# Performance work log

Hardware: AMD Instinct MI355X
Metric: run time of the kernel (lower is better)

The kernel has to match this reference:

```python
import jax, jax.numpy as jnp
import numpy as np

N_U, N_R, D, H, E = 100000, 50000, 128, 64, 1000000


def setup_inputs() -> dict:
    key = jax.random.key(0)
    ks = jax.random.split(key, 12)
    s = 1.0 / np.sqrt(D)
    return {
        "x_user": jax.random.normal(ks[0], (N_U, D), jnp.float32),
        "x_res": jax.random.normal(ks[1], (N_R, D), jnp.float32),
        "edge_ua_src": jax.random.randint(ks[2], (E,), 0, N_U),
        "edge_ua_dst": jax.random.randint(ks[3], (E,), 0, N_R),
        "edge_ru_src": jax.random.randint(ks[4], (E,), 0, N_R),
        "edge_ru_dst": jax.random.randint(ks[5], (E,), 0, N_U),
        "W_l_ua": jax.random.normal(ks[6], (D, H), jnp.float32) * s,
        "b_ua": jax.random.normal(ks[7], (H,), jnp.float32) * s,
        "W_r_ua": jax.random.normal(ks[8], (D, H), jnp.float32) * s,
        "W_l_ru": jax.random.normal(ks[9], (D, H), jnp.float32) * s,
        "b_ru": jax.random.normal(ks[10], (H,), jnp.float32) * s,
        "W_r_ru": jax.random.normal(ks[11], (D, H), jnp.float32) * s,
    }


def _sage(x_src, x_dst, src, dst, n_dst, W_l, b_l, W_r):
    # gather neighbor feats, scatter-mean onto dst nodes (0 for isolated nodes)
    agg = jax.ops.segment_sum(x_src[src], dst, num_segments=n_dst)  # [n_dst, D]
    cnt = jax.ops.segment_sum(jnp.ones((src.shape[0], 1), x_src.dtype), dst,
                              num_segments=n_dst)
    mean = agg / jnp.maximum(cnt, 1.0)
    # SAGEConv: lin_l(mean neighbor) + bias + lin_r(self), no bias on lin_r
    return mean @ W_l + b_l + x_dst @ W_r


def reference(x_user, x_res, edge_ua_src, edge_ua_dst, edge_ru_src, edge_ru_dst,
              W_l_ua, b_ua, W_r_ua, W_l_ru, b_ru, W_r_ru):
    out_res = jax.nn.relu(_sage(x_user, x_res, edge_ua_src, edge_ua_dst, N_R,
                                W_l_ua, b_ua, W_r_ua))
    out_user = jax.nn.relu(_sage(x_res, x_user, edge_ru_src, edge_ru_dst, N_U,
                                 W_l_ru, b_ru, W_r_ru))
    return out_user, out_res
```

## Files before the change

### kernel.cpp

```cpp
#include <hip/hip_runtime.h>

#define N_U 100000
#define N_R 50000
#define DIM 128
#define HID 64
#define NE  1000000

#define BROWS 128
#define NB_R ((N_R + 127) / 128)
#define NB_U ((N_U + 127) / 128)
#define NBKT (NB_R + NB_U)
#define N_TOT (N_R + N_U)
#define MAXB 800
#define CHUNK 4096
#define BINGRID ((NE + CHUNK - 1) / CHUNK)
#define NBIN (2 * BINGRID)
#define CAPR 3072
#define CAPU 1536
#define RCAP 48
#define GU2 ((N_U + 127) / 128)
#define GR2 ((N_R + 127) / 128)
#define NPROJ (GU2 + GR2)
#define NPREP (NBIN + NPROJ)
#define TRIPLE (3 * NBIN)
#define LDSU 9856
#define NGATH (2 * NB_R + 2 * NB_U)

typedef unsigned int uint;
typedef __attribute__((ext_vector_type(8))) short      bf16x8;
typedef __attribute__((ext_vector_type(4))) float      f32x4;
typedef __attribute__((ext_vector_type(2))) float      f32x2;
typedef __attribute__((ext_vector_type(8))) unsigned short u16x8;

__device__ inline uint bf16_rne(float f) {
    uint u = __float_as_uint(f);
    u += 0x7FFFu + ((u >> 16) & 1u);
    return u >> 16;
}
__device__ inline float bf_lo(uint v) { return __uint_as_float(v << 16); }
__device__ inline float bf_hi(uint v) { return __uint_as_float(v & 0xFFFF0000u); }

__device__ inline uint cvt_pk_bf16(float lo, float hi) {
    uint r;
    asm("v_cvt_pk_bf16_f32 %0, %1, %2" : "=v"(r) : "v"(lo), "v"(hi));
    return r;
}

__device__ inline void pk_acc(f32x2& acc, uint v) {
    f32x2 val;
    val[0] = __uint_as_float(v << 16);
    val[1] = __uint_as_float(v & 0xFFFF0000u);
    asm("v_pk_add_f32 %0, %1, %2" : "+v"(acc) : "v"(val));
}

__device__ inline int bucket_base(int b) {
    return (b < NB_R) ? b * CAPR : NB_R * CAPR + (b - NB_R) * CAPU;
}

__global__ __launch_bounds__(256) void wcvt_kernel(
    const float* __restrict__ Wlua, const float* __restrict__ Wlru,
    const float* __restrict__ Wrua, const float* __restrict__ Wrru,
    unsigned short* __restrict__ Wbf, int* __restrict__ cur)
{
    if (blockIdx.x < 4) {
        const float* Ws[4] = {Wlua, Wlru, Wrua, Wrru};
        const float* W = Ws[blockIdx.x];
        unsigned short* dst = Wbf + blockIdx.x * 8192;
        for (int i = threadIdx.x; i < 1024; i += 256) {
            int k8 = i >> 6, col = i & 63;
            u16x8 p;
#pragma unroll
            for (int j = 0; j < 8; ++j)
                p[j] = (unsigned short)bf16_rne(W[(k8 * 8 + j) * HID + col]);
            *(u16x8*)&dst[i * 8] = p;
        }
    } else {
        int i = (blockIdx.x - 4) * 256 + threadIdx.x;
        if (i < NBKT) cur[i] = 0;
    }
}

__global__ __launch_bounds__(512, 4) void prep_kernel(
    const int* __restrict__ srcA, const int* __restrict__ dstA,
    const int* __restrict__ srcB, const int* __restrict__ dstB,
    int* __restrict__ cur, int* __restrict__ rec,
    const float* __restrict__ xu, const float* __restrict__ xr,
    const unsigned short* __restrict__ Wbf,
    const float* __restrict__ b_ua, const float* __restrict__ b_ru,
    uint* __restrict__ h_user, uint* __restrict__ h_res,
    uint* __restrict__ sbuf)
{
    __shared__ __align__(16) uint lds[LDSU];

    const int bid = blockIdx.x;
    const int t = threadIdx.x;
    int binid = -1, projid = -1;
    if (bid < TRIPLE) {
        if (bid % 3 == 0) binid = bid / 3;
        else projid = (bid / 3) * 2 + (bid % 3 - 1);
    } else {
        projid = 2 * NBIN + (bid - TRIPLE);
    }

    if (binid >= 0) {
        int* cntL = (int*)lds;
        int* offL = cntL + MAXB;
        int* curL = offL + MAXB;
        int* gbase = curL + MAXB;
        int* srec = gbase + MAXB;
        unsigned short* sbkt = (unsigned short*)(lds + 7296);
        int* tmp = (int*)(lds + 9344);

        const int seg = (binid >= BINGRID) ? 1 : 0;
        const int blk = binid - seg * BINGRID;
        const int* __restrict__ src = seg ? srcB : srcA;
        const int* __restrict__ dst = seg ? dstB : dstA;
        const int nbkt   = seg ? NB_U : NB_R;
        const int bktOff = seg ? NB_R : 0;

        const int e0 = blk * CHUNK;
        const int nhere = min(CHUNK, NE - e0);

        for (int i = t; i < nbkt; i += 512) cntL[i] = 0;
        __syncthreads();

        int myB[8], myR[8];
#pragma unroll
        for (int l = 0; l < 8; ++l) {
            int i = e0 + l * 512 + t;
            if (i < NE) {
                int d = dst[i];
                myB[l] = d >> 7;
                myR[l] = ((d & 127) << 17) | src[i];
                atomicAdd(&cntL[myB[l]], 1);
            } else myB[l] = -1;
        }
        __syncthreads();

        int vals[4], s = 0;
#pragma unroll
        for (int l = 0; l < 4; ++l) {
            int idx = t * 4 + l;
            vals[l] = (idx < nbkt) ? cntL[idx] : 0;
            s += vals[l];
        }
        tmp[t] = s;
        __syncthreads();
        for (int o = 1; o < 512; o <<= 1) {
            int v = (t >= o) ? tmp[t - o] : 0;
            __syncthreads();
            tmp[t] += v;
            __syncthreads();
        }
        int run = tmp[t] - s;
#pragma unroll
        for (int l = 0; l < 4; ++l) {
            int idx = t * 4 + l;
            if (idx < nbkt) { offL[idx] = run; curL[idx] = run; }
            run += vals[l];
        }
        __syncthreads();

        for (int i = t; i < nbkt; i += 512)
            if (cntL[i] > 0)
                gbase[i] = bucket_base(bktOff + i) + atomicAdd(&cur[bktOff + i], cntL[i]);

#pragma unroll
        for (int l = 0; l < 8; ++l) {
            if (myB[l] >= 0) {
                int slot = atomicAdd(&curL[myB[l]], 1);
                srec[slot] = myR[l];
                sbkt[slot] = (unsigned short)myB[l];
            }
        }
        __syncthreads();

        for (int sI = t; sI < nhere; sI += 512) {
            int b = sbkt[sI];
            rec[gbase[b] + (sI - offL[b])] = srec[sI];
        }
        return;
    }

    int blk, nrows;
    const float *x, *bias;
    const unsigned short *w0g, *w1g;
    uint* hb; uint* sb;
    if (projid < GU2) {
        blk = projid; x = xu; w0g = Wbf; w1g = Wbf + 3 * 8192; bias = b_ru;
        hb = h_user; sb = sbuf; nrows = N_U;
    } else {
        blk = projid - GU2; x = xr; w0g = Wbf + 1 * 8192; w1g = Wbf + 2 * 8192;
        bias = b_ua; hb = h_res; sb = sbuf + (size_t)N_U * 32; nrows = N_R;
    }

    const int rowbase = blk * 128;

    {
        const uint4* s0 = (const uint4*)w0g;
        const uint4* s1 = (const uint4*)w1g;
        uint4* d0 = (uint4*)lds;
        uint4* d1 = (uint4*)(lds + 4096);
        for (int i = t; i < 1024; i += 512) { d0[i] = s0[i]; d1[i] = s1[i]; }
    }

    const int wv = t >> 6, l = t & 63;
    const int lrow = l & 15, lk = l >> 4;
    const int myrow = rowbase + wv * 16 + lrow;
    const bool valid = myrow < nrows;
    const float4* xp = (const float4*)(x + (size_t)myrow * DIM + lk * 8);

    float4 z = make_float4(0.f, 0.f, 0.f, 0.f);
    float4 x0a = z, x0b = z, x1a = z, x1b = z, x2a = z, x2b = z, x3a = z, x3b = z;
    if (valid) {
        x0a = xp[0];  x0b = xp[1];
        x1a = xp[8];  x1b = xp[9];
        x2a = xp[16]; x2b = xp[17];
        x3a = xp[24]; x3b = xp[25];
    }
    __syncthreads();

    f32x4 acc0[4], acc1[4];
#pragma unroll
    for (int n = 0; n < 4; ++n) { acc0[n] = (f32x4)0.f; acc1[n] = (f32x4)0.f; }

#define KKSTEP(KK, XA, XB)                                                        \
    {                                                                             \
        union { uint4 u; bf16x8 v; } af;                                          \
        af.u.x = cvt_pk_bf16(XA.x, XA.y);                                         \
        af.u.y = cvt_pk_bf16(XA.z, XA.w);                                         \
        af.u.z = cvt_pk_bf16(XB.x, XB.y);                                         \
        af.u.w = cvt_pk_bf16(XB.z, XB.w);                                         \
        const int k8 = KK * 4 + lk;                                               \
        _Pragma("unroll")                                                         \
        for (int n = 0; n < 4; ++n) {                                             \
            const int col = n * 16 + lrow;                                        \
            bf16x8 b0 = *(const bf16x8*)&lds[(k8 * 64 + col) * 4];                \
            bf16x8 b1 = *(const bf16x8*)&lds[4096 + (k8 * 64 + col) * 4];         \
            acc0[n] = __builtin_amdgcn_mfma_f32_16x16x32_bf16(af.v, b0, acc0[n], 0, 0, 0); \
            acc1[n] = __builtin_amdgcn_mfma_f32_16x16x32_bf16(af.v, b1, acc1[n], 0, 0, 0); \
        }                                                                         \
    }
    KKSTEP(0, x0a, x0b)
    KKSTEP(1, x1a, x1b)
    KKSTEP(2, x2a, x2b)
    KKSTEP(3, x3a, x3b)
#undef KKSTEP

#pragma unroll
    for (int n = 0; n < 4; ++n) {
        float bv = bias[n * 16 + lrow];
#pragma unroll
        for (int r = 0; r < 4; ++r) acc1[n][r] += bv;
    }

    __syncthreads();
    uint* hA = lds;
    uint* hS = lds + 4608;
#pragma unroll
    for (int n = 0; n < 4; ++n) {
#pragma unroll
        for (int r = 0; r < 4; ++r) {
            int row = wv * 16 + lk * 4 + r;
            float hm = acc0[n][r], ho = __shfl_xor(hm, 1);
            float sm = acc1[n][r], so = __shfl_xor(sm, 1);
            if (!(lrow & 1)) {
                int c2 = n * 8 + (lrow >> 1);
                hA[row * 36 + c2] = cvt_pk_bf16(hm, ho);
                hS[row * 36 + c2] = cvt_pk_bf16(sm, so);
            }
        }
    }
    __syncthreads();
    for (int i = t; i < 128 * 8; i += 512) {
        int r = i >> 3, q = i & 7;
        if (rowbase + r < nrows) {
            *(uint4*)(hb + (size_t)(rowbase + r) * 32 + q * 4) =
                *(const uint4*)&hA[r * 36 + q * 4];
            *(uint4*)(sb + (size_t)(rowbase + r) * 32 + q * 4) =
                *(const uint4*)&hS[r * 36 + q * 4];
        }
    }
}

__global__ __launch_bounds__(256) void csr_gather_kernel(
    const int* __restrict__ rec, const int* __restrict__ cur,
    const uint* __restrict__ hu, const uint* __restrict__ hr,
    const uint* __restrict__ sbuf, float* __restrict__ out)
{
    __shared__ int srecB[64 * RCAP];
    __shared__ int cntL[64];

    const int t = threadIdx.x;
    const int blk = blockIdx.x;
    int bkt, half, nrows;
    size_t rowOff;
    const uint* __restrict__ h;
    if (blk < 2 * NB_R) {
        bkt = blk >> 1; half = blk & 1;
        h = hu; rowOff = N_U; nrows = N_R;
    } else {
        int u = blk - 2 * NB_R;
        bkt = NB_R + (u >> 1); half = u & 1;
        h = hr; rowOff = 0; nrows = N_U;
    }
    const int lbase = ((bkt < NB_R) ? bkt * 128 : (bkt - NB_R) * 128) + half * 64;
    if (lbase >= nrows) return;

    const int rbase = bucket_base(bkt);
    const int rcnt  = min(cur[bkt], (bkt < NB_R) ? CAPR : CAPU);
    const int rlo   = half * 64;

    if (t < 64) cntL[t] = 0;
    __syncthreads();
    for (int i = t; i < rcnt; i += 256) {
        int r = rec[rbase + i];
        int lr = (r >> 17) - rlo;
        if ((unsigned)lr < 64u) {
            int slot = atomicAdd(&cntL[lr], 1);
            if (slot < RCAP) srecB[lr * RCAP + slot] = r;
        }
    }
    __syncthreads();

    const int team = t >> 5, l32 = t & 31;
    const int q  = l32 >> 3;
    const int cl = l32 & 7;

    for (int rr = team; rr < 64; rr += 8) {
        const int lr = lbase + rr;
        if (lr >= nrows) continue;
        const int d = min(cntL[rr], RCAP);
        const int base = rr * RCAP;
        const uint* srow = sbuf + (rowOff + lr) * 32;
        float* orow = out + (rowOff + lr) * 64;

        float s0 = 0.f, s1 = 0.f, s2 = 0.f, s3 = 0.f;
        float s4 = 0.f, s5 = 0.f, s6 = 0.f, s7 = 0.f;
        if (l32 < 8) {
            uint4 sv = *(const uint4*)(srow + cl * 4);
            s0 = bf_lo(sv.x); s1 = bf_hi(sv.x); s2 = bf_lo(sv.y); s3 = bf_hi(sv.y);
            s4 = bf_lo(sv.z); s5 = bf_hi(sv.z); s6 = bf_lo(sv.w); s7 = bf_hi(sv.w);
        }

        f32x2 A0 = {0.f, 0.f}, A1 = {0.f, 0.f}, A2 = {0.f, 0.f}, A3 = {0.f, 0.f};
#define ACC(v) { pk_acc(A0, v.x); pk_acc(A1, v.y); pk_acc(A2, v.z); pk_acc(A3, v.w); }
        const uint4 z4 = make_uint4(0u, 0u, 0u, 0u);
        for (int j = 0; j < d; j += 16) {
            uint4 v0 = z4, v1 = z4, v2 = z4, v3 = z4;
            if (j + q < d)
                v0 = *(const uint4*)(h + (size_t)(srecB[base + j + q] & 0x1FFFF) * 32 + cl * 4);
            if (j + 4 + q < d)
                v1 = *(const uint4*)(h + (size_t)(srecB[base + j + 4 + q] & 0x1FFFF) * 32 + cl * 4);
            if (j + 8 + q < d)
                v2 = *(const uint4*)(h + (size_t)(srecB[base + j + 8 + q] & 0x1FFFF) * 32 + cl * 4);
            if (j + 12 + q < d)
                v3 = *(const uint4*)(h + (size_t)(srecB[base + j + 12 + q] & 0x1FFFF) * 32 + cl * 4);
            ACC(v0) ACC(v1) ACC(v2) ACC(v3)
        }
#undef ACC

#pragma unroll
        for (int off = 8; off <= 16; off <<= 1) {
            A0[0] += __shfl_xor(A0[0], off); A0[1] += __shfl_xor(A0[1], off);
            A1[0] += __shfl_xor(A1[0], off); A1[1] += __shfl_xor(A1[1], off);
            A2[0] += __shfl_xor(A2[0], off); A2[1] += __shfl_xor(A2[1], off);
            A3[0] += __shfl_xor(A3[0], off); A3[1] += __shfl_xor(A3[1], off);
        }

        if (l32 < 8) {
            float invd = 1.0f / fmaxf((float)d, 1.0f);
            float4 rA, rB;
            rA.x = fmaxf(A0[0] * invd + s0, 0.f);
            rA.y = fmaxf(A0[1] * invd + s1, 0.f);
            rA.z = fmaxf(A1[0] * invd + s2, 0.f);
            rA.w = fmaxf(A1[1] * invd + s3, 0.f);
            rB.x = fmaxf(A2[0] * invd + s4, 0.f);
            rB.y = fmaxf(A2[1] * invd + s5, 0.f);
            rB.z = fmaxf(A3[0] * invd + s6, 0.f);
            rB.w = fmaxf(A3[1] * invd + s7, 0.f);
            *(float4*)(orow + cl * 8) = rA;
            *(float4*)(orow + cl * 8 + 4) = rB;
        }
    }
}

extern "C" void kernel_launch(void* const* d_in, const int* in_sizes, int n_in,
                              void* d_out, int out_size, void* d_ws, size_t ws_size,
                              hipStream_t stream)
{
    const float* x_user = (const float*)d_in[0];
    const float* x_res  = (const float*)d_in[1];
    const int* ua_src   = (const int*)d_in[2];
    const int* ua_dst   = (const int*)d_in[3];
    const int* ru_src   = (const int*)d_in[4];
    const int* ru_dst   = (const int*)d_in[5];
    const float* W_l_ua = (const float*)d_in[6];
    const float* b_ua   = (const float*)d_in[7];
    const float* W_r_ua = (const float*)d_in[8];
    const float* W_l_ru = (const float*)d_in[9];
    const float* b_ru   = (const float*)d_in[10];
    const float* W_r_ru = (const float*)d_in[11];

    uint* h_user = (uint*)d_ws;
    uint* h_res  = h_user + (size_t)N_U * 32;
    uint* sbuf   = h_res + (size_t)N_R * 32;
    unsigned short* Wbf = (unsigned short*)(sbuf + (size_t)N_TOT * 32);
    int*  cur    = (int*)(Wbf + 4 * 8192);
    int*  rec    = cur + NBKT;

    wcvt_kernel<<<4 + (NBKT + 255) / 256, 256, 0, stream>>>(
        W_l_ua, W_l_ru, W_r_ua, W_r_ru, Wbf, cur);

    prep_kernel<<<NPREP, 512, 0, stream>>>(
        ua_src, ua_dst, ru_src, ru_dst, cur, rec,
        x_user, x_res, Wbf, b_ua, b_ru, h_user, h_res, sbuf);

    csr_gather_kernel<<<NGATH, 256, 0, stream>>>(
        rec, cur, h_user, h_res, sbuf, (float*)d_out);
}
```

Measured before the change: 89.79 us.

## Convert prep and gather kernels to persistent blocks with atomic work queues

Both the prep kernel and the CSR gather kernel now launch a fixed grid of persistent blocks. Each block repeatedly pulls the next logical block index from a global atomic counter, which is zeroed alongside the bucket cursors. This is meant to cut block launch and tail overhead and to balance uneven work such as variable-degree gather rows. It adds one atomic and two barriers per work item, and the rec buffer moves by two ints.

```diff
diff --git a/kernel.cpp b/kernel.cpp
--- a/kernel.cpp
+++ b/kernel.cpp
@@ -25,6 +25,8 @@
 #define TRIPLE (3 * NBIN)
 #define LDSU 9856
 #define NGATH (2 * NB_R + 2 * NB_U)
+#define PGRID 1024
+#define GGRID 2048
 
 typedef unsigned int uint;
 typedef __attribute__((ext_vector_type(8))) short      bf16x8;
@@ -76,14 +78,14 @@
         }
     } else {
         int i = (blockIdx.x - 4) * 256 + threadIdx.x;
-        if (i < NBKT) cur[i] = 0;
+        if (i < NBKT + 2) cur[i] = 0;
     }
 }
 
 __global__ __launch_bounds__(512, 4) void prep_kernel(
     const int* __restrict__ srcA, const int* __restrict__ dstA,
     const int* __restrict__ srcB, const int* __restrict__ dstB,
-    int* __restrict__ cur, int* __restrict__ rec,
+    int* __restrict__ cur, int* __restrict__ rec, int* __restrict__ pcnt,
     const float* __restrict__ xu, const float* __restrict__ xr,
     const unsigned short* __restrict__ Wbf,
     const float* __restrict__ b_ua, const float* __restrict__ b_ru,
@@ -91,296 +93,313 @@
     uint* __restrict__ sbuf)
 {
     __shared__ __align__(16) uint lds[LDSU];
-
-    const int bid = blockIdx.x;
+    __shared__ int sbid;
     const int t = threadIdx.x;
-    int binid = -1, projid = -1;
-    if (bid < TRIPLE) {
-        if (bid % 3 == 0) binid = bid / 3;
-        else projid = (bid / 3) * 2 + (bid % 3 - 1);
-    } else {
-        projid = 2 * NBIN + (bid - TRIPLE);
-    }
-
-    if (binid >= 0) {
-        int* cntL = (int*)lds;
-        int* offL = cntL + MAXB;
-        int* curL = offL + MAXB;
-        int* gbase = curL + MAXB;
-        int* srec = gbase + MAXB;
-        unsigned short* sbkt = (unsigned short*)(lds + 7296);
-        int* tmp = (int*)(lds + 9344);
-
-        const int seg = (binid >= BINGRID) ? 1 : 0;
-        const int blk = binid - seg * BINGRID;
-        const int* __restrict__ src = seg ? srcB : srcA;
-        const int* __restrict__ dst = seg ? dstB : dstA;
-        const int nbkt   = seg ? NB_U : NB_R;
-        const int bktOff = seg ? NB_R : 0;
-
-        const int e0 = blk * CHUNK;
-        const int nhere = min(CHUNK, NE - e0);
-
-        for (int i = t; i < nbkt; i += 512) cntL[i] = 0;
-        __syncthreads();
-
-        int myB[8], myR[8];
-#pragma unroll
-        for (int l = 0; l < 8; ++l) {
-            int i = e0 + l * 512 + t;
-            if (i < NE) {
-                int d = dst[i];
-                myB[l] = d >> 7;
-                myR[l] = ((d & 127) << 17) | src[i];
-                atomicAdd(&cntL[myB[l]], 1);
-            } else myB[l] = -1;
-        }
-        __syncthreads();
-
-        int vals[4], s = 0;
-#pragma unroll
-        for (int l = 0; l < 4; ++l) {
-            int idx = t * 4 + l;
-            vals[l] = (idx < nbkt) ? cntL[idx] : 0;
-            s += vals[l];
-        }
-        tmp[t] = s;
-        __syncthreads();
-        for (int o = 1; o < 512; o <<= 1) {
-            int v = (t >= o) ? tmp[t - o] : 0;
+
+    for (;;) {
+        __syncthreads();
+        if (t == 0) sbid = atomicAdd(pcnt, 1);
+        __syncthreads();
+        const int bid = sbid;
+        if (bid >= NPREP) return;
+
+        int binid = -1, projid = -1;
+        if (bid < TRIPLE) {
+            if (bid % 3 == 0) binid = bid / 3;
+            else projid = (bid / 3) * 2 + (bid % 3 - 1);
+        } else {
+            projid = 2 * NBIN + (bid - TRIPLE);
+        }
+
+        if (binid >= 0) {
+            int* cntL = (int*)lds;
+            int* offL = cntL + MAXB;
+            int* curL = offL + MAXB;
+            int* gbase = curL + MAXB;
+            int* srec = gbase + MAXB;
+            unsigned short* sbkt = (unsigned short*)(lds + 7296);
+            int* tmp = (int*)(lds + 9344);
+
+            const int seg = (binid >= BINGRID) ? 1 : 0;
+            const int blk = binid - seg * BINGRID;
+            const int* __restrict__ src = seg ? srcB : srcA;
+            const int* __restrict__ dst = seg ? dstB : dstA;
+            const int nbkt   = seg ? NB_U : NB_R;
+            const int bktOff = seg ? NB_R : 0;
+
+            const int e0 = blk * CHUNK;
+            const int nhere = min(CHUNK, NE - e0);
+
+            for (int i = t; i < nbkt; i += 512) cntL[i] = 0;
             __syncthreads();
-            tmp[t] += v;
+
+            int myB[8], myR[8];
+#pragma unroll
+            for (int l = 0; l < 8; ++l) {
+                int i = e0 + l * 512 + t;
+                if (i < NE) {
+                    int d = dst[i];
+                    myB[l] = d >> 7;
+                    myR[l] = ((d & 127) << 17) | src[i];
+                    atomicAdd(&cntL[myB[l]], 1);
+                } else myB[l] = -1;
+            }
             __syncthreads();
-        }
-        int run = tmp[t] - s;
-#pragma unroll
-        for (int l = 0; l < 4; ++l) {
-            int idx = t * 4 + l;
-            if (idx < nbkt) { offL[idx] = run; curL[idx] = run; }
-            run += vals[l];
-        }
-        __syncthreads();
-
-        for (int i = t; i < nbkt; i += 512)
-            if (cntL[i] > 0)
-                gbase[i] = bucket_base(bktOff + i) + atomicAdd(&cur[bktOff + i], cntL[i]);
-
-#pragma unroll
-        for (int l = 0; l < 8; ++l) {
-            if (myB[l] >= 0) {
-                int slot = atomicAdd(&curL[myB[l]], 1);
-                srec[slot] = myR[l];
-                sbkt[slot] = (unsigned short)myB[l];
-            }
-        }
-        __syncthreads();
-
-        for (int sI = t; sI < nhere; sI += 512) {
-            int b = sbkt[sI];
-            rec[gbase[b] + (sI - offL[b])] = srec[sI];
-        }
-        return;
-    }
-
-    int blk, nrows;
-    const float *x, *bias;
-    const unsigned short *w0g, *w1g;
-    uint* hb; uint* sb;
-    if (projid < GU2) {
-        blk = projid; x = xu; w0g = Wbf; w1g = Wbf + 3 * 8192; bias = b_ru;
-        hb = h_user; sb = sbuf; nrows = N_U;
-    } else {
-        blk = projid - GU2; x = xr; w0g = Wbf + 1 * 8192; w1g = Wbf + 2 * 8192;
-        bias = b_ua; hb = h_res; sb = sbuf + (size_t)N_U * 32; nrows = N_R;
-    }
-
-    const int rowbase = blk * 128;
-
-    {
-        const uint4* s0 = (const uint4*)w0g;
-        const uint4* s1 = (const uint4*)w1g;
-        uint4* d0 = (uint4*)lds;
-        uint4* d1 = (uint4*)(lds + 4096);
-        for (int i = t; i < 1024; i += 512) { d0[i] = s0[i]; d1[i] = s1[i]; }
-    }
-
-    const int wv = t >> 6, l = t & 63;
-    const int lrow = l & 15, lk = l >> 4;
-    const int myrow = rowbase + wv * 16 + lrow;
-    const bool valid = myrow < nrows;
-    const float4* xp = (const float4*)(x + (size_t)myrow * DIM + lk * 8);
-
-    float4 z = make_float4(0.f, 0.f, 0.f, 0.f);
-    float4 x0a = z, x0b = z, x1a = z, x1b = z, x2a = z, x2b = z, x3a = z, x3b = z;
-    if (valid) {
-        x0a = xp[0];  x0b = xp[1];
-        x1a = xp[8];  x1b = xp[9];
-        x2a = xp[16]; x2b = xp[17];
-        x3a = xp[24]; x3b = xp[25];
-    }
-    __syncthreads();
-
-    f32x4 acc0[4], acc1[4];
-#pragma unroll
-    for (int n = 0; n < 4; ++n) { acc0[n] = (f32x4)0.f; acc1[n] = (f32x4)0.f; }
+
+            int vals[4], s = 0;
+#pragma unroll
+            for (int l = 0; l < 4; ++l) {
+                int idx = t * 4 + l;
+                vals[l] = (idx < nbkt) ? cntL[idx] : 0;
+                s += vals[l];
+            }
+            tmp[t] = s;
+            __syncthreads();
+            for (int o = 1; o < 512; o <<= 1) {
+                int v = (t >= o) ? tmp[t - o] : 0;
+                __syncthreads();
+                tmp[t] += v;
+                __syncthreads();
+            }
+            int run = tmp[t] - s;
+#pragma unroll
+            for (int l = 0; l < 4; ++l) {
+                int idx = t * 4 + l;
+                if (idx < nbkt) { offL[idx] = run; curL[idx] = run; }
+                run += vals[l];
+            }
+            __syncthreads();
+
+            for (int i = t; i < nbkt; i += 512)
+                if (cntL[i] > 0)
+                    gbase[i] = bucket_base(bktOff + i) + atomicAdd(&cur[bktOff + i], cntL[i]);
+
+#pragma unroll
+            for (int l = 0; l < 8; ++l) {
+                if (myB[l] >= 0) {
+                    int slot = atomicAdd(&curL[myB[l]], 1);
+                    srec[slot] = myR[l];
+                    sbkt[slot] = (unsigned short)myB[l];
+                }
+            }
+            __syncthreads();
+
+            for (int sI = t; sI < nhere; sI += 512) {
+                int b = sbkt[sI];
+                rec[gbase[b] + (sI - offL[b])] = srec[sI];
+            }
+            continue;
+        }
+
+        int blk, nrows;
+        const float *x, *bias;
+        const unsigned short *w0g, *w1g;
+        uint* hb; uint* sb;
+        if (projid < GU2) {
+            blk = projid; x = xu; w0g = Wbf; w1g = Wbf + 3 * 8192; bias = b_ru;
+            hb = h_user; sb = sbuf; nrows = N_U;
+        } else {
+            blk = projid - GU2; x = xr; w0g = Wbf + 1 * 8192; w1g = Wbf + 2 * 8192;
+            bias = b_ua; hb = h_res; sb = sbuf + (size_t)N_U * 32; nrows = N_R;
+        }
+
+        const int rowbase = blk * 128;
+
+        {
+            const uint4* s0 = (const uint4*)w0g;
+            const uint4* s1 = (const uint4*)w1g;
+            uint4* d0 = (uint4*)lds;
+            uint4* d1 = (uint4*)(lds + 4096);
+            for (int i = t; i < 1024; i += 512) { d0[i] = s0[i]; d1[i] = s1[i]; }
+        }
+
+        const int wv = t >> 6, l = t & 63;
+        const int lrow = l & 15, lk = l >> 4;
+        const int myrow = rowbase + wv * 16 + lrow;
+        const bool valid = myrow < nrows;
+        const float4* xp = (const float4*)(x + (size_t)myrow * DIM + lk * 8);
+
+        float4 z = make_float4(0.f, 0.f, 0.f, 0.f);
+        float4 x0a = z, x0b = z, x1a = z, x1b = z, x2a = z, x2b = z, x3a = z, x3b = z;
+        if (valid) {
+            x0a = xp[0];  x0b = xp[1];
+            x1a = xp[8];  x1b = xp[9];
+            x2a = xp[16]; x2b = xp[17];
+            x3a = xp[24]; x3b = xp[25];
+        }
+        __syncthreads();
+
+        f32x4 acc0[4], acc1[4];
+#pragma unroll
+        for (int n = 0; n < 4; ++n) { acc0[n] = (f32x4)0.f; acc1[n] = (f32x4)0.f; }
 
 #define KKSTEP(KK, XA, XB)                                                        \
-    {                                                                             \
-        union { uint4 u; bf16x8 v; } af;                                          \
-        af.u.x = cvt_pk_bf16(XA.x, XA.y);                                         \
-        af.u.y = cvt_pk_bf16(XA.z, XA.w);                                         \
-        af.u.z = cvt_pk_bf16(XB.x, XB.y);                                         \
-        af.u.w = cvt_pk_bf16(XB.z, XB.w);                                         \
-        const int k8 = KK * 4 + lk;                                               \
-        _Pragma("unroll")                                                         \
-        for (int n = 0; n < 4; ++n) {                                             \
-            const int col = n * 16 + lrow;                                        \
-            bf16x8 b0 = *(const bf16x8*)&lds[(k8 * 64 + col) * 4];                \
-            bf16x8 b1 = *(const bf16x8*)&lds[4096 + (k8 * 64 + col) * 4];         \
-            acc0[n] = __builtin_amdgcn_mfma_f32_16x16x32_bf16(af.v, b0, acc0[n], 0, 0, 0); \
-            acc1[n] = __builtin_amdgcn_mfma_f32_16x16x32_bf16(af.v, b1, acc1[n], 0, 0, 0); \
-        }                                                                         \
-    }
-    KKSTEP(0, x0a, x0b)
-    KKSTEP(1, x1a, x1b)
-    KKSTEP(2, x2a, x2b)
-    KKSTEP(3, x3a, x3b)
+        {                                                                         \
+            union { uint4 u; bf16x8 v; } af;                                      \
+            af.u.x = cvt_pk_bf16(XA.x, XA.y);                                     \
+            af.u.y = cvt_pk_bf16(XA.z, XA.w);                                     \
+            af.u.z = cvt_pk_bf16(XB.x, XB.y);                                     \
+            af.u.w = cvt_pk_bf16(XB.z, XB.w);                                     \
+            const int k8 = KK * 4 + lk;                                           \
+            _Pragma("unroll")                                                     \
+            for (int n = 0; n < 4; ++n) {                                         \
+                const int col = n * 16 + lrow;                                    \
+                bf16x8 b0 = *(const bf16x8*)&lds[(k8 * 64 + col) * 4];            \
+                bf16x8 b1 = *(const bf16x8*)&lds[4096 + (k8 * 64 + col) * 4];     \
+                acc0[n] = __builtin_amdgcn_mfma_f32_16x16x32_bf16(af.v, b0, acc0[n], 0, 0, 0); \
+                acc1[n] = __builtin_amdgcn_mfma_f32_16x16x32_bf16(af.v, b1, acc1[n], 0, 0, 0); \
+            }                                                                     \
+        }
+        KKSTEP(0, x0a, x0b)
+        KKSTEP(1, x1a, x1b)
+        KKSTEP(2, x2a, x2b)
+        KKSTEP(3, x3a, x3b)
 #undef KKSTEP
 
 #pragma unroll
-    for (int n = 0; n < 4; ++n) {
-        float bv = bias[n * 16 + lrow];
-#pragma unroll
-        for (int r = 0; r < 4; ++r) acc1[n][r] += bv;
-    }
-
-    __syncthreads();
-    uint* hA = lds;
-    uint* hS = lds + 4608;
-#pragma unroll
-    for (int n = 0; n < 4; ++n) {
-#pragma unroll
-        for (int r = 0; r < 4; ++r) {
-            int row = wv * 16 + lk * 4 + r;
-            float hm = acc0[n][r], ho = __shfl_xor(hm, 1);
-            float sm = acc1[n][r], so = __shfl_xor(sm, 1);
-            if (!(lrow & 1)) {
-                int c2 = n * 8 + (lrow >> 1);
-                hA[row * 36 + c2] = cvt_pk_bf16(hm, ho);
-                hS[row * 36 + c2] = cvt_pk_bf16(sm, so);
-            }
-        }
-    }
-    __syncthreads();
-    for (int i = t; i < 128 * 8; i += 512) {
-        int r = i >> 3, q = i & 7;
-        if (rowbase + r < nrows) {
-            *(uint4*)(hb + (size_t)(rowbase + r) * 32 + q * 4) =
-                *(const uint4*)&hA[r * 36 + q * 4];
-            *(uint4*)(sb + (size_t)(rowbase + r) * 32 + q * 4) =
-                *(const uint4*)&hS[r * 36 + q * 4];
+        for (int n = 0; n < 4; ++n) {
+            float bv = bias[n * 16 + lrow];
+#pragma unroll
+            for (int r = 0; r < 4; ++r) acc1[n][r] += bv;
+        }
+
+        __syncthreads();
+        uint* hA = lds;
+        uint* hS = lds + 4608;
+#pragma unroll
+        for (int n = 0; n < 4; ++n) {
+#pragma unroll
+            for (int r = 0; r < 4; ++r) {
+                int row = wv * 16 + lk * 4 + r;
+                float hm = acc0[n][r], ho = __shfl_xor(hm, 1);
+                float sm = acc1[n][r], so = __shfl_xor(sm, 1);
+                if (!(lrow & 1)) {
+                    int c2 = n * 8 + (lrow >> 1);
+                    hA[row * 36 + c2] = cvt_pk_bf16(hm, ho);
+                    hS[row * 36 + c2] = cvt_pk_bf16(sm, so);
+                }
+            }
+        }
+        __syncthreads();
+        for (int i = t; i < 128 * 8; i += 512) {
+            int r = i >> 3, q = i & 7;
+            if (rowbase + r < nrows) {
+                *(uint4*)(hb + (size_t)(rowbase + r) * 32 + q * 4) =
+                    *(const uint4*)&hA[r * 36 + q * 4];
+                *(uint4*)(sb + (size_t)(rowbase + r) * 32 + q * 4) =
+                    *(const uint4*)&hS[r * 36 + q * 4];
+            }
         }
     }
 }
 
 __global__ __launch_bounds__(256) void csr_gather_kernel(
     const int* __restrict__ rec, const int* __restrict__ cur,
+    int* __restrict__ gcnt,
     const uint* __restrict__ hu, const uint* __restrict__ hr,
     const uint* __restrict__ sbuf, float* __restrict__ out)
 {
     __shared__ int srecB[64 * RCAP];
     __shared__ int cntL[64];
-
+    __shared__ int sbid;
     const int t = threadIdx.x;
-    const int blk = blockIdx.x;
-    int bkt, half, nrows;
-    size_t rowOff;
-    const uint* __restrict__ h;
-    if (blk < 2 * NB_R) {
-        bkt = blk >> 1; half = blk & 1;
-        h = hu; rowOff = N_U; nrows = N_R;
-    } else {
-        int u = blk - 2 * NB_R;
-        bkt = NB_R + (u >> 1); half = u & 1;
-        h = hr; rowOff = 0; nrows = N_U;
-    }
-    const int lbase = ((bkt < NB_R) ? bkt * 128 : (bkt - NB_R) * 128) + half * 64;
-    if (lbase >= nrows) return;
-
-    const int rbase = bucket_base(bkt);
-    const int rcnt  = min(cur[bkt], (bkt < NB_R) ? CAPR : CAPU);
-    const int rlo   = half * 64;
-
-    if (t < 64) cntL[t] = 0;
-    __syncthreads();
-    for (int i = t; i < rcnt; i += 256) {
-        int r = rec[rbase + i];
-        int lr = (r >> 17) - rlo;
-        if ((unsigned)lr < 64u) {
-            int slot = atomicAdd(&cntL[lr], 1);
-            if (slot < RCAP) srecB[lr * RCAP + slot] = r;
-        }
-    }
-    __syncthreads();
-
-    const int team = t >> 5, l32 = t & 31;
-    const int q  = l32 >> 3;
-    const int cl = l32 & 7;
-
-    for (int rr = team; rr < 64; rr += 8) {
-        const int lr = lbase + rr;
-        if (lr >= nrows) continue;
-        const int d = min(cntL[rr], RCAP);
-        const int base = rr * RCAP;
-        const uint* srow = sbuf + (rowOff + lr) * 32;
-        float* orow = out + (rowOff + lr) * 64;
-
-        float s0 = 0.f, s1 = 0.f, s2 = 0.f, s3 = 0.f;
-        float s4 = 0.f, s5 = 0.f, s6 = 0.f, s7 = 0.f;
-        if (l32 < 8) {
-            uint4 sv = *(const uint4*)(srow + cl * 4);
-            s0 = bf_lo(sv.x); s1 = bf_hi(sv.x); s2 = bf_lo(sv.y); s3 = bf_hi(sv.y);
-            s4 = bf_lo(sv.z); s5 = bf_hi(sv.z); s6 = bf_lo(sv.w); s7 = bf_hi(sv.w);
-        }
-
-        f32x2 A0 = {0.f, 0.f}, A1 = {0.f, 0.f}, A2 = {0.f, 0.f}, A3 = {0.f, 0.f};
+
+    for (;;) {
+        __syncthreads();
+        if (t == 0) sbid = atomicAdd(gcnt, 1);
+        __syncthreads();
+        const int blk = sbid;
+        if (blk >= NGATH) return;
+
+        int bkt, half, nrows;
+        size_t rowOff;
+        const uint* __restrict__ h;
+        if (blk < 2 * NB_R) {
+            bkt = blk >> 1; half = blk & 1;
+            h = hu; rowOff = N_U; nrows = N_R;
+        } else {
+            int u = blk - 2 * NB_R;
+            bkt = NB_R + (u >> 1); half = u & 1;
+            h = hr; rowOff = 0; nrows = N_U;
+        }
+        const int lbase = ((bkt < NB_R) ? bkt * 128 : (bkt - NB_R) * 128) + half * 64;
+        if (lbase >= nrows) continue;
+
+        const int rbase = bucket_base(bkt);
+        const int rcnt  = min(cur[bkt], (bkt < NB_R) ? CAPR : CAPU);
+        const int rlo   = half * 64;
+
+        if (t < 64) cntL[t] = 0;
+        __syncthreads();
+        for (int i = t; i < rcnt; i += 256) {
+            int r = rec[rbase + i];
+            int lr = (r >> 17) - rlo;
+            if ((unsigned)lr < 64u) {
+                int slot = atomicAdd(&cntL[lr], 1);
+                if (slot < RCAP) srecB[lr * RCAP + slot] = r;
+            }
+        }
+        __syncthreads();
+
+        const int team = t >> 5, l32 = t & 31;
+        const int q  = l32 >> 3;
+        const int cl = l32 & 7;
+
+        for (int rr = team; rr < 64; rr += 8) {
+            const int lr = lbase + rr;
+            if (lr >= nrows) continue;
+            const int d = min(cntL[rr], RCAP);
+            const int base = rr * RCAP;
+            const uint* srow = sbuf + (rowOff + lr) * 32;
+            float* orow = out + (rowOff + lr) * 64;
+
+            float s0 = 0.f, s1 = 0.f, s2 = 0.f, s3 = 0.f;
+            float s4 = 0.f, s5 = 0.f, s6 = 0.f, s7 = 0.f;
+            if (l32 < 8) {
+                uint4 sv = *(const uint4*)(srow + cl * 4);
+                s0 = bf_lo(sv.x); s1 = bf_hi(sv.x); s2 = bf_lo(sv.y); s3 = bf_hi(sv.y);
+                s4 = bf_lo(sv.z); s5 = bf_hi(sv.z); s6 = bf_lo(sv.w); s7 = bf_hi(sv.w);
+            }
+
+            f32x2 A0 = {0.f, 0.f}, A1 = {0.f, 0.f}, A2 = {0.f, 0.f}, A3 = {0.f, 0.f};
 #define ACC(v) { pk_acc(A0, v.x); pk_acc(A1, v.y); pk_acc(A2, v.z); pk_acc(A3, v.w); }
-        const uint4 z4 = make_uint4(0u, 0u, 0u, 0u);
-        for (int j = 0; j < d; j += 16) {
-            uint4 v0 = z4, v1 = z4, v2 = z4, v3 = z4;
-            if (j + q < d)
-                v0 = *(const uint4*)(h + (size_t)(srecB[base + j + q] & 0x1FFFF) * 32 + cl * 4);
-            if (j + 4 + q < d)
-                v1 = *(const uint4*)(h + (size_t)(srecB[base + j + 4 + q] & 0x1FFFF) * 32 + cl * 4);
-            if (j + 8 + q < d)
-                v2 = *(const uint4*)(h + (size_t)(srecB[base + j + 8 + q] & 0x1FFFF) * 32 + cl * 4);
-            if (j + 12 + q < d)
-                v3 = *(const uint4*)(h + (size_t)(srecB[base + j + 12 + q] & 0x1FFFF) * 32 + cl * 4);
-            ACC(v0) ACC(v1) ACC(v2) ACC(v3)
-        }
+            const uint4 z4 = make_uint4(0u, 0u, 0u, 0u);
+            for (int j = 0; j < d; j += 16) {
+                uint4 v0 = z4, v1 = z4, v2 = z4, v3 = z4;
+                if (j + q < d)
+                    v0 = *(const uint4*)(h + (size_t)(srecB[base + j + q] & 0x1FFFF) * 32 + cl * 4);
+                if (j + 4 + q < d)
+                    v1 = *(const uint4*)(h + (size_t)(srecB[base + j + 4 + q] & 0x1FFFF) * 32 + cl * 4);
+                if (j + 8 + q < d)
+                    v2 = *(const uint4*)(h + (size_t)(srecB[base + j + 8 + q] & 0x1FFFF) * 32 + cl * 4);
+                if (j + 12 + q < d)
+                    v3 = *(const uint4*)(h + (size_t)(srecB[base + j + 12 + q] & 0x1FFFF) * 32 + cl * 4);
+                ACC(v0) ACC(v1) ACC(v2) ACC(v3)
+            }
 #undef ACC
 
 #pragma unroll
-        for (int off = 8; off <= 16; off <<= 1) {
-            A0[0] += __shfl_xor(A0[0], off); A0[1] += __shfl_xor(A0[1], off);
-            A1[0] += __shfl_xor(A1[0], off); A1[1] += __shfl_xor(A1[1], off);
-            A2[0] += __shfl_xor(A2[0], off); A2[1] += __shfl_xor(A2[1], off);
-            A3[0] += __shfl_xor(A3[0], off); A3[1] += __shfl_xor(A3[1], off);
-        }
-
-        if (l32 < 8) {
-            float invd = 1.0f / fmaxf((float)d, 1.0f);
-            float4 rA, rB;
-            rA.x = fmaxf(A0[0] * invd + s0, 0.f);
-            rA.y = fmaxf(A0[1] * invd + s1, 0.f);
-            rA.z = fmaxf(A1[0] * invd + s2, 0.f);
-            rA.w = fmaxf(A1[1] * invd + s3, 0.f);
-            rB.x = fmaxf(A2[0] * invd + s4, 0.f);
-            rB.y = fmaxf(A2[1] * invd + s5, 0.f);
-            rB.z = fmaxf(A3[0] * invd + s6, 0.f);
-            rB.w = fmaxf(A3[1] * invd + s7, 0.f);
-            *(float4*)(orow + cl * 8) = rA;
-            *(float4*)(orow + cl * 8 + 4) = rB;
+            for (int off = 8; off <= 16; off <<= 1) {
+                A0[0] += __shfl_xor(A0[0], off); A0[1] += __shfl_xor(A0[1], off);
+                A1[0] += __shfl_xor(A1[0], off); A1[1] += __shfl_xor(A1[1], off);
+                A2[0] += __shfl_xor(A2[0], off); A2[1] += __shfl_xor(A2[1], off);
+                A3[0] += __shfl_xor(A3[0], off); A3[1] += __shfl_xor(A3[1], off);
+            }
+
+            if (l32 < 8) {
+                float invd = 1.0f / fmaxf((float)d, 1.0f);
+                float4 rA, rB;
+                rA.x = fmaxf(A0[0] * invd + s0, 0.f);
+                rA.y = fmaxf(A0[1] * invd + s1, 0.f);
+                rA.z = fmaxf(A1[0] * invd + s2, 0.f);
+                rA.w = fmaxf(A1[1] * invd + s3, 0.f);
+                rB.x = fmaxf(A2[0] * invd + s4, 0.f);
+                rB.y = fmaxf(A2[1] * invd + s5, 0.f);
+                rB.z = fmaxf(A3[0] * invd + s6, 0.f);
+                rB.w = fmaxf(A3[1] * invd + s7, 0.f);
+                *(float4*)(orow + cl * 8) = rA;
+                *(float4*)(orow + cl * 8 + 4) = rB;
+            }
         }
     }
 }
@@ -407,15 +426,17 @@
     uint* sbuf   = h_res + (size_t)N_R * 32;
     unsigned short* Wbf = (unsigned short*)(sbuf + (size_t)N_TOT * 32);
     int*  cur    = (int*)(Wbf + 4 * 8192);
-    int*  rec    = cur + NBKT;
-
-    wcvt_kernel<<<4 + (NBKT + 255) / 256, 256, 0, stream>>>(
+    int*  pcnt   = cur + NBKT;
+    int*  gcnt   = pcnt + 1;
+    int*  rec    = gcnt + 1;
+
+    wcvt_kernel<<<4 + (NBKT + 2 + 255) / 256, 256, 0, stream>>>(
         W_l_ua, W_l_ru, W_r_ua, W_r_ru, Wbf, cur);
 
-    prep_kernel<<<NPREP, 512, 0, stream>>>(
-        ua_src, ua_dst, ru_src, ru_dst, cur, rec,
+    prep_kernel<<<PGRID, 512, 0, stream>>>(
+        ua_src, ua_dst, ru_src, ru_dst, cur, rec, pcnt,
         x_user, x_res, Wbf, b_ua, b_ru, h_user, h_res, sbuf);
 
-    csr_gather_kernel<<<NGATH, 256, 0, stream>>>(
-        rec, cur, h_user, h_res, sbuf, (float*)d_out);
-}
+    csr_gather_kernel<<<GGRID, 256, 0, stream>>>(
+        rec, cur, gcnt, h_user, h_res, sbuf, (float*)d_out);
+}
```

New measurement: 134.8 us. +50.1%, slower.
